# Optimization experiments

Hardware: AMD Instinct MI355X
Metric: run time of the kernel (lower is better)

## Reference

```python
import jax, jax.numpy as jnp
import numpy as np

N = 5000        # graph nodes
DEG = 16        # fixed out-degree -> 1-hop neighborhood size S = DEG+1
S = DEG + 1
T = 10          # n_templates
MN = 10         # n_templates_nodes
D = 128         # n_features
EPS = 0.1       # entropic regularization of the OT solver
N_OUTER = 3     # FGW outer (gradient/linearization) iterations
N_SINK = 5      # Sinkhorn projections per outer iteration


def setup_inputs() -> dict:
    key = jax.random.key(0)
    k1, k2, k3, k4 = jax.random.split(key, 4)
    x = jax.random.normal(k1, (N, D), jnp.float32)
    dst = jax.random.randint(k2, (N * DEG,), 0, N)
    src = jnp.repeat(jnp.arange(N), DEG)
    edge_index = jnp.stack([src, dst])  # [2, E], node i's neighbors are rows i*DEG:(i+1)*DEG
    tmpl = jax.random.uniform(k3, (T, MN, MN), jnp.float32)
    templates = 0.5 * (tmpl + jnp.swapaxes(tmpl, 1, 2))  # symmetric init, as in template_initialisation
    templates_features = 0.001 * jax.random.normal(k4, (T, MN, D), jnp.float32)
    q0 = jnp.zeros((T, MN), jnp.float32)
    alpha0 = jnp.zeros((1,), jnp.float32)
    return {"x": x, "edge_index": edge_index, "templates": templates,
            "templates_features": templates_features, "q0": q0, "alpha0": alpha0}


def _ltfgw(x, edge_index, templates, templates_features, q0, alpha0):
    alpha = jax.nn.sigmoid(alpha0)[0]
    C2 = jax.nn.softmax(templates, axis=1)        # [T,m,m] template structure (softmax over dim=1 as in forward)
    q = jax.nn.softmax(q0, axis=1)                # [T,m] template node weights
    dst = edge_index[1].reshape(N, DEG)           # neighbor list per node
    nodes_local = jnp.concatenate([jnp.arange(N)[:, None], dst], axis=1)  # [N,S] 1-hop neighborhood
    # local adjacency C1[n,a,b] = 1 iff edge between local nodes a,b (symmetrized, no self loop)
    neigh_all = dst[nodes_local]                  # [N,S,DEG]
    adj = (neigh_all[:, :, None, :] == nodes_local[:, None, :, None]).any(-1)
    adj = adj | jnp.swapaxes(adj, 1, 2)
    C1 = adj.astype(x.dtype) * (1.0 - jnp.eye(S, dtype=x.dtype))
    p = jnp.full((S,), 1.0 / S, dtype=x.dtype)    # uniform local node weights
    F2 = templates_features
    xl = x[nodes_local]                           # [N,S,D]
    # feature cost M[n,t,s,m] = ||xl[n,s] - F2[t,m]||^2
    M = ((xl ** 2).sum(-1)[:, None, :, None] + (F2 ** 2).sum(-1)[None, :, None, :]
         - 2.0 * jnp.einsum('nsd,tmd->ntsm', xl, F2))
    # GW (square loss) constant terms
    hC1 = jnp.einsum('nij,j->ni', C1 ** 2, p)
    hC2 = jnp.einsum('tij,tj->ti', C2 ** 2, q)
    constC = hC1[:, None, :, None] + hC2[None, :, None, :]   # [N,T,S,m]
    log_p = jnp.log(p)[None, None, :]
    log_q = jnp.log(q)[None, :, :]
    G = (p[None, None, :, None] * q[None, :, None, :]) * jnp.ones((N, 1, 1, 1), x.dtype)

    def outer(G, _):
        tens = constC - 2.0 * jnp.einsum('nij,ntjk,tlk->ntil', C1, G, C2)
        cost = (1.0 - alpha) * M + 2.0 * alpha * tens        # FGW gradient = linearized cost
        logK = -cost / EPS
        def sink(ab, _):
            a, b = ab
            a = log_p - jax.nn.logsumexp(logK + b[:, :, None, :], axis=-1)
            b = log_q - jax.nn.logsumexp(logK + a[..., None], axis=-2)
            return (a, b), None
        init = (jnp.zeros((N, T, S), x.dtype), jnp.zeros((N, T, MN), x.dtype))
        (a, b), _ = jax.lax.scan(sink, init, None, length=N_SINK)
        return jnp.exp(logK + a[..., None] + b[:, :, None, :]), None

    G, _ = jax.lax.scan(outer, G, None, length=N_OUTER)
    tens = constC - 2.0 * jnp.einsum('nij,ntjk,tlk->ntil', C1, G, C2)
    # FGW value per (node, template): (1-a)<M,G> + a<constC - 2 C1 G C2^T, G>
    dist = jnp.sum(G * ((1.0 - alpha) * M + alpha * tens), axis=(-2, -1))
    return dist  # [N, T]


def reference(x, edge_index, templates, templates_features, q0, alpha0):
    return _ltfgw(x, edge_index, templates, templates_features, q0, alpha0)
```

## Files before the change

kernel.cpp:

```cpp
#include <hip/hip_runtime.h>
#include <math.h>

#define NN   5000
#define DEG  16
#define S    17
#define T    10
#define MN   10
#define D    128
#define NOUT 3
#define NSK  5

#define WPB   8
#define BLOCK (WPB * 64)
#define NEG   -3.0e38f
#define LOG2E 1.44269504088896f
#define LN2   0.69314718055995f
#define TINY  1e-30f

typedef unsigned uint2v __attribute__((ext_vector_type(2)));

__device__ __forceinline__ float fast_rcp(float x) { return __builtin_amdgcn_rcpf(x); }

#if __has_builtin(__builtin_amdgcn_exp2f)
__device__ __forceinline__ float fast_exp2(float x) { return __builtin_amdgcn_exp2f(x); }
#else
__device__ __forceinline__ float fast_exp2(float x) { return __expf(x * LN2); }
#endif

template <int CTRL>
__device__ __forceinline__ float dpp_movf(float v) {
    return __int_as_float(__builtin_amdgcn_update_dpp(
        0, __float_as_int(v), CTRL, 0xF, 0xF, true));
}
__device__ __forceinline__ float rowsum16(float v) {
    v += dpp_movf<0x121>(v);
    v += dpp_movf<0x122>(v);
    v += dpp_movf<0x124>(v);
    v += dpp_movf<0x128>(v);
    return v;
}
__device__ __forceinline__ float rowmax16(float v) {
    v = fmaxf(v, dpp_movf<0x121>(v));
    v = fmaxf(v, dpp_movf<0x122>(v));
    v = fmaxf(v, dpp_movf<0x124>(v));
    v = fmaxf(v, dpp_movf<0x128>(v));
    return v;
}

__device__ __forceinline__ float bfly16(float v) {
#if __has_builtin(__builtin_amdgcn_permlane16_swap)
    uint2v r = __builtin_amdgcn_permlane16_swap(__float_as_uint(v), __float_as_uint(v),
                                                false, false);
    return __uint_as_float(r[0]) + __uint_as_float(r[1]);
#else
    return v + __int_as_float(__builtin_amdgcn_ds_swizzle(__float_as_int(v), 0x401F));
#endif
}
__device__ __forceinline__ float bfly32(float v) {
#if __has_builtin(__builtin_amdgcn_permlane32_swap)
    uint2v r = __builtin_amdgcn_permlane32_swap(__float_as_uint(v), __float_as_uint(v),
                                                false, false);
    return __uint_as_float(r[0]) + __uint_as_float(r[1]);
#else
    return v + __shfl_xor(v, 32, 64);
#endif
}

__device__ __forceinline__ float dot10(const float* __restrict__ row,
                                       const float* __restrict__ cr) {
    float4 a = *(const float4*)(row);
    float4 b = *(const float4*)(row + 4);
    float2 c = *(const float2*)(row + 8);
    float e0 = fmaf(cr[1], a.y, cr[0] * a.x);
    float e1 = fmaf(cr[3], a.w, cr[2] * a.z);
    float e2 = fmaf(cr[5], b.y, cr[4] * b.x);
    float e3 = fmaf(cr[7], b.w, cr[6] * b.z);
    float e4 = fmaf(cr[9], c.y, cr[8] * c.x);
    return ((e0 + e1) + (e2 + e3)) + e4;
}

__global__ __launch_bounds__(320) void ltfgw_pre(
    const float* __restrict__ x,
    const int*   __restrict__ edge,
    const float* __restrict__ F2,
    float*       __restrict__ wsMp,
    unsigned*    __restrict__ wsMask,
    float*       __restrict__ wsSqF2)
{
    const int n   = blockIdx.x;
    const int tid = threadIdx.x;
    const int* dst = edge + NN * DEG;

    if (n == NN) {
        if (tid < T * MN) {
            const float4* fr = (const float4*)(F2 + (size_t)tid * D);
            float acc = 0.f;
            #pragma unroll 8
            for (int i = 0; i < D / 4; ++i) {
                float4 f = fr[i];
                acc += f.x*f.x + f.y*f.y + f.z*f.z + f.w*f.w;
            }
            wsSqF2[tid] = acc;
        }
        return;
    }

    __shared__ int      loc[S];
    __shared__ int      neigh[S][DEG];
    __shared__ unsigned cm[S];
    __shared__ float    xsq_s;

    if (tid < S) { loc[tid] = (tid == 0) ? n : dst[n * DEG + tid - 1]; cm[tid] = 0u; }
    __syncthreads();

    if (tid < S * DEG) neigh[tid >> 4][tid & 15] = dst[loc[tid >> 4] * DEG + (tid & 15)];
    if (tid < 64) {
        float v0 = x[(size_t)n * D + tid];
        float v1 = x[(size_t)n * D + 64 + tid];
        float pp = v0 * v0 + v1 * v1;
        pp = rowsum16(pp);
        pp += __shfl_xor(pp, 16, 64);
        pp += __shfl_xor(pp, 32, 64);
        if (tid == 0) xsq_s = pp;
    }
    __syncthreads();

    if (tid < S * S) {
        int a = tid / S, b = tid % S;
        int la = loc[a], lb = loc[b];
        bool adj = false;
        #pragma unroll
        for (int k = 0; k < DEG; ++k) adj = adj | (neigh[a][k] == lb) | (neigh[b][k] == la);
        if (a != b && adj) atomicOr(&cm[a], 1u << b);
    }
    __syncthreads();

    if (tid < S) wsMask[n * S + tid] = cm[tid];
    if (tid >= 32 && tid < 32 + T * MN) {
        int c = tid - 32;
        const float4* fr = (const float4*)(F2 + (size_t)c * D);
        const float4* xr = (const float4*)(x + (size_t)n * D);
        float dotv = 0.f;
        #pragma unroll 8
        for (int d4 = 0; d4 < D / 4; ++d4) {
            float4 f = fr[d4], xv = xr[d4];
            dotv += f.x*xv.x + f.y*xv.y + f.z*xv.z + f.w*xv.w;
        }
        wsMp[n * (T * MN) + c] = xsq_s - 2.f * dotv;
    }
}

__global__ __launch_bounds__(BLOCK) void ltfgw_wave(
    const int*      __restrict__ edge,
    const float*    __restrict__ tmpl,
    const float*    __restrict__ q0,
    const float*    __restrict__ alpha0,
    const float*    __restrict__ wsMp,
    const unsigned* __restrict__ wsMask,
    const float*    __restrict__ wsSqF2,
    float*          __restrict__ out)
{
    const int tid  = threadIdx.x;
    const int w    = tid >> 6;
    const int gid  = blockIdx.x * WPB + w;
    const int n    = gid / T;
    const int t    = gid - n * T;
    const int lane = tid & 63;
    const int q    = lane >> 4;
    const int m    = lane & 15;
    const bool act = (m < MN);
    const int mc   = act ? m : (MN - 1);

    __shared__ __align__(16) float C2l[WPB][MN][17];
    __shared__ __align__(16) float GL[WPB][19][16];
    __shared__ __align__(16) float QL[WPB][16];

    const int* dst = edge + NN * DEG;

    float vq = q0[t * MN + mc];
    float zq = act ? vq : NEG;
    float mq = rowmax16(zq);
    float sq = rowsum16(__expf(zq - mq));
    const float qm = __expf(vq - (mq + __logf(sq)));
    if (q == 0) QL[w][m] = act ? qm : 0.f;
    if (act && q == 0) {
        float v[MN]; float cmx = NEG;
        #pragma unroll
        for (int i = 0; i < MN; ++i) { v[i] = tmpl[t * MN * MN + i * MN + m]; cmx = fmaxf(cmx, v[i]); }
        float ssum = 0.f;
        #pragma unroll
        for (int i = 0; i < MN; ++i) { v[i] = __expf(v[i] - cmx); ssum += v[i]; }
        float inv = fast_rcp(ssum);
        #pragma unroll
        for (int i = 0; i < MN; ++i) C2l[w][i][m] = v[i] * inv;
    }

    int sr[5];
    #pragma unroll
    for (int r = 0; r < 5; ++r) { int s0 = q + 4 * r; sr[r] = (s0 > 16) ? 16 : s0; }
    unsigned msk[5]; float npop[5]; float Mp[5];
    const int cidx = t * MN + mc;
    #pragma unroll
    for (int r = 0; r < 5; ++r) {
        int lr  = (sr[r] == 0) ? n : dst[n * DEG + sr[r] - 1];
        msk[r]  = wsMask[n * S + sr[r]];
        npop[r] = (float)__popc(msk[r]);
        Mp[r]   = wsMp[lr * (T * MN) + cidx];
    }
    const float sqf2c = wsSqF2[cidx];

    float crReg[MN];
    #pragma unroll
    for (int k = 0; k < MN; ++k) crReg[k] = C2l[w][mc][k];

    float hC2 = 0.f, qC2m = 0.f;
    {
        float ql[MN];
        #pragma unroll
        for (int k = 0; k < MN; ++k) ql[k] = QL[w][k];
        #pragma unroll
        for (int k = 0; k < MN; ++k) {
            float cq = crReg[k] * ql[k];
            qC2m += cq;
            hC2  = fmaf(crReg[k], cq, hC2);
        }
    }

    const float alpha = fast_rcp(1.f + __expf(-alpha0[0]));
    const float oma   = 1.f - alpha;
    const float p_    = 1.f / (float)S;
    const float fa42  = 40.f * alpha * LOG2E;
    const float qop   = qm * (float)S;
    const unsigned exm = act ? 0x1FFFEu : 0u;
    const int j16  = (q == 0) ? 16 : 18;

    float lkP2b[5], rm2[5];
    {
        const float nl2e10 = -10.f * LOG2E;
        #pragma unroll
        for (int r = 0; r < 5; ++r) {
            float M_ = Mp[r] + sqf2c;
            float cC = npop[r] * p_ + hC2;
            float lk2 = nl2e10 * (oma * M_ + 2.f * alpha * cC);
            rm2[r]   = rowmax16(act ? lk2 : NEG) + 14.4f;
            lkP2b[r] = act ? (lk2 - rm2[r]) : NEG;
        }
    }

    float tens[5], Kt[5], ub[5], v_, G[5];
    {
        float pq = p_ * qC2m;
        #pragma unroll
        for (int r = 0; r < 5; ++r) tens[r] = pq * npop[r];
    }

    for (int o = 1; o <= NOUT; ++o) {
        #pragma unroll
        for (int r = 0; r < 5; ++r)
            Kt[r] = fast_exp2(fmaf(fa42, tens[r], lkP2b[r]));
        float Kt4c = (q == 0) ? Kt[4] : 0.f;

        #pragma unroll
        for (int r = 0; r < 5; ++r) ub[r] = fast_rcp(rowsum16(Kt[r]));
        {
            float a0 = Kt[0] * ub[0], a1 = Kt[1] * ub[1];
            float a2 = Kt[2] * ub[2], a3 = Kt[3] * ub[3];
            float a4 = fmaf(Kt4c, ub[4], TINY);
            float cs = ((a0 + a1) + (a2 + a3)) + a4;
            cs = bfly16(cs); cs = bfly32(cs);
            v_ = qop * fast_rcp(cs);
        }
        #pragma unroll
        for (int it = 1; it < NSK; ++it) {
            #pragma unroll
            for (int r = 0; r < 5; ++r)
                ub[r] = fast_rcp(rowsum16(Kt[r] * v_));
            float a0 = Kt[0] * ub[0], a1 = Kt[1] * ub[1];
            float a2 = Kt[2] * ub[2], a3 = Kt[3] * ub[3];
            float a4 = fmaf(Kt4c, ub[4], TINY);
            float cs = ((a0 + a1) + (a2 + a3)) + a4;
            cs = bfly16(cs); cs = bfly32(cs);
            v_ = qop * fast_rcp(cs);
        }
        float pv = p_ * v_;
        #pragma unroll
        for (int r = 0; r < 5; ++r) G[r] = Kt[r] * ub[r] * pv;

        #pragma unroll
        for (int r = 0; r < 4; ++r) GL[w][q + 4*r][m] = G[r];
        GL[w][j16][m] = G[4];
        float cg = (G[0] + G[1]) + (G[2] + G[3]) + ((q == 0) ? G[4] : 0.f);
        cg = bfly16(cg); cg = bfly32(cg);
        if (q == 0) GL[w][17][m] = cg;
        float Fm = dot10(&GL[w][17][0], crReg);
        float H0 = dot10(&GL[w][0][0],  crReg);
        #pragma unroll
        for (int r = 0; r < 5; ++r) {
            unsigned ex = msk[r] & exm;
            if (r == 0) ex = (q == 0) ? 0u : ex;
            float tn = H0;
            while (ex) {
                int j = __builtin_ctz(ex);
                ex &= ex - 1u;
                tn += dot10(&GL[w][j][0], crReg);
            }
            tens[r] = tn;
        }
        if (q == 0) tens[0] = Fm - H0;
    }

    float val = 0.f;
    #pragma unroll
    for (int r = 0; r < 5; ++r) {
        float cC = npop[r] * p_ + hC2;
        float lk2r = lkP2b[r] + rm2[r];
        float integ = -(0.1f * LN2) * lk2r - alpha * cC - 2.f * alpha * tens[r];
        bool valid = act && (r < 4 || q == 0);
        val += valid ? G[r] * integ : 0.f;
    }
    val = rowsum16(val);
    val = bfly16(val);
    val = bfly32(val);
    if (lane == 0) out[n * T + t] = val;
}

extern "C" void kernel_launch(void* const* d_in, const int* in_sizes, int n_in,
                              void* d_out, int out_size, void* d_ws, size_t ws_size,
                              hipStream_t stream) {
    const float* x      = (const float*)d_in[0];
    const int*   edge   = (const int*)  d_in[1];
    const float* tmpl   = (const float*)d_in[2];
    const float* F2     = (const float*)d_in[3];
    const float* q0     = (const float*)d_in[4];
    const float* alpha0 = (const float*)d_in[5];
    float*       out    = (float*)d_out;

    float*    wsMp    = (float*)d_ws;
    unsigned* wsMask  = (unsigned*)((char*)d_ws + (size_t)NN * T * MN * 4);
    float*    wsSqF2  = (float*)((char*)d_ws + (size_t)NN * T * MN * 4 + (size_t)NN * S * 4);

    hipLaunchKernelGGL(ltfgw_pre, dim3(NN + 1), dim3(320), 0, stream,
                       x, edge, F2, wsMp, wsMask, wsSqF2);
    hipLaunchKernelGGL(ltfgw_wave, dim3(NN * T / WPB), dim3(BLOCK), 0, stream,
                       edge, tmpl, q0, alpha0, wsMp, wsMask, wsSqF2, out);
}
```

Measured before the change: 219.3 us.

## Pack two node-template problems per wavefront using 32-lane halves

Each 64-lane wavefront now solves two (node, template) FGW problems, one per 32-lane half, with 9 rows per lane instead of 5. The grid is halved and cross-lane reductions drop the 32-lane butterfly step. The row-max values are moved into shared memory to save registers. The cost is more registers per lane for the larger row arrays and a longer serial chain of work per lane, which can lower occupancy.

```diff
diff --git a/kernel.cpp b/kernel.cpp
--- a/kernel.cpp
+++ b/kernel.cpp
@@ -11,7 +11,9 @@
 #define NSK  5
 
 #define WPB   8
+#define PPW   2
 #define BLOCK (WPB * 64)
+#define RS    9
 #define NEG   -3.0e38f
 #define LOG2E 1.44269504088896f
 #define LN2   0.69314718055995f
@@ -54,15 +56,6 @@
     return __uint_as_float(r[0]) + __uint_as_float(r[1]);
 #else
     return v + __int_as_float(__builtin_amdgcn_ds_swizzle(__float_as_int(v), 0x401F));
-#endif
-}
-__device__ __forceinline__ float bfly32(float v) {
-#if __has_builtin(__builtin_amdgcn_permlane32_swap)
-    uint2v r = __builtin_amdgcn_permlane32_swap(__float_as_uint(v), __float_as_uint(v),
-                                                false, false);
-    return __uint_as_float(r[0]) + __uint_as_float(r[1]);
-#else
-    return v + __shfl_xor(v, 32, 64);
 #endif
 }
 
@@ -162,18 +155,22 @@
 {
     const int tid  = threadIdx.x;
     const int w    = tid >> 6;
-    const int gid  = blockIdx.x * WPB + w;
-    const int n    = gid / T;
-    const int t    = gid - n * T;
     const int lane = tid & 63;
+    const int half = lane >> 5;
     const int q    = lane >> 4;
+    const int ql   = q & 1;
     const int m    = lane & 15;
     const bool act = (m < MN);
     const int mc   = act ? m : (MN - 1);
-
-    __shared__ __align__(16) float C2l[WPB][MN][17];
-    __shared__ __align__(16) float GL[WPB][19][16];
-    __shared__ __align__(16) float QL[WPB][16];
+    const bool pad8 = (ql == 1);
+    const int gid  = (blockIdx.x * WPB + w) * PPW + half;
+    const int n    = gid / T;
+    const int t    = gid - n * T;
+
+    __shared__ __align__(16) float C2l[WPB][PPW][MN][17];
+    __shared__ __align__(16) float GL [WPB][PPW][19][16];
+    __shared__ __align__(16) float QL [WPB][PPW][16];
+    __shared__               float RM [WPB][PPW][20];
 
     const int* dst = edge + NN * DEG;
 
@@ -182,8 +179,8 @@
     float mq = rowmax16(zq);
     float sq = rowsum16(__expf(zq - mq));
     const float qm = __expf(vq - (mq + __logf(sq)));
-    if (q == 0) QL[w][m] = act ? qm : 0.f;
-    if (act && q == 0) {
+    if (ql == 0) QL[w][half][m] = act ? qm : 0.f;
+    if (act && ql == 0) {
         float v[MN]; float cmx = NEG;
         #pragma unroll
         for (int i = 0; i < MN; ++i) { v[i] = tmpl[t * MN * MN + i * MN + m]; cmx = fmaxf(cmx, v[i]); }
@@ -192,35 +189,33 @@
         for (int i = 0; i < MN; ++i) { v[i] = __expf(v[i] - cmx); ssum += v[i]; }
         float inv = fast_rcp(ssum);
         #pragma unroll
-        for (int i = 0; i < MN; ++i) C2l[w][i][m] = v[i] * inv;
-    }
-
-    int sr[5];
-    #pragma unroll
-    for (int r = 0; r < 5; ++r) { int s0 = q + 4 * r; sr[r] = (s0 > 16) ? 16 : s0; }
-    unsigned msk[5]; float npop[5]; float Mp[5];
+        for (int i = 0; i < MN; ++i) C2l[w][half][i][m] = v[i] * inv;
+    }
+
+    unsigned msk[RS]; float Mp[RS];
     const int cidx = t * MN + mc;
     #pragma unroll
-    for (int r = 0; r < 5; ++r) {
-        int lr  = (sr[r] == 0) ? n : dst[n * DEG + sr[r] - 1];
-        msk[r]  = wsMask[n * S + sr[r]];
-        npop[r] = (float)__popc(msk[r]);
+    for (int r = 0; r < RS; ++r) {
+        int s   = 2 * r + ql; s = (s > 16) ? 16 : s;
+        int lr  = (s == 0) ? n : dst[n * DEG + s - 1];
+        msk[r]  = wsMask[n * S + s];
         Mp[r]   = wsMp[lr * (T * MN) + cidx];
     }
+    if (pad8) msk[8] = 0u;
     const float sqf2c = wsSqF2[cidx];
 
     float crReg[MN];
     #pragma unroll
-    for (int k = 0; k < MN; ++k) crReg[k] = C2l[w][mc][k];
+    for (int k = 0; k < MN; ++k) crReg[k] = C2l[w][half][mc][k];
 
     float hC2 = 0.f, qC2m = 0.f;
     {
-        float ql[MN];
-        #pragma unroll
-        for (int k = 0; k < MN; ++k) ql[k] = QL[w][k];
+        float ql_[MN];
+        #pragma unroll
+        for (int k = 0; k < MN; ++k) ql_[k] = QL[w][half][k];
         #pragma unroll
         for (int k = 0; k < MN; ++k) {
-            float cq = crReg[k] * ql[k];
+            float cq = crReg[k] * ql_[k];
             qC2m += cq;
             hC2  = fmaf(crReg[k], cq, hC2);
         }
@@ -232,96 +227,100 @@
     const float fa42  = 40.f * alpha * LOG2E;
     const float qop   = qm * (float)S;
     const unsigned exm = act ? 0x1FFFEu : 0u;
-    const int j16  = (q == 0) ? 16 : 18;
-
-    float lkP2b[5], rm2[5];
+
+    float lkP2b[RS];
     {
         const float nl2e10 = -10.f * LOG2E;
         #pragma unroll
-        for (int r = 0; r < 5; ++r) {
-            float M_ = Mp[r] + sqf2c;
-            float cC = npop[r] * p_ + hC2;
+        for (int r = 0; r < RS; ++r) {
+            int s = 2 * r + ql; s = (s > 16) ? 16 : s;
+            float M_  = Mp[r] + sqf2c;
+            float cC  = (float)__popc(msk[r]) * p_ + hC2;
             float lk2 = nl2e10 * (oma * M_ + 2.f * alpha * cC);
-            rm2[r]   = rowmax16(act ? lk2 : NEG) + 14.4f;
-            lkP2b[r] = act ? (lk2 - rm2[r]) : NEG;
-        }
-    }
-
-    float tens[5], Kt[5], ub[5], v_, G[5];
+            float rm2 = rowmax16(act ? lk2 : NEG) + 14.4f;
+            bool vld  = !(pad8 && r == 8);
+            lkP2b[r]  = (act && vld) ? (lk2 - rm2) : NEG;
+            if (m == 0 && vld) RM[w][half][s] = rm2;
+        }
+    }
+
+    float tens[RS], Kt[RS], ub[RS], v_, G[RS];
     {
         float pq = p_ * qC2m;
         #pragma unroll
-        for (int r = 0; r < 5; ++r) tens[r] = pq * npop[r];
+        for (int r = 0; r < RS; ++r) tens[r] = pq * (float)__popc(msk[r]);
     }
 
     for (int o = 1; o <= NOUT; ++o) {
         #pragma unroll
-        for (int r = 0; r < 5; ++r)
+        for (int r = 0; r < RS; ++r)
             Kt[r] = fast_exp2(fmaf(fa42, tens[r], lkP2b[r]));
-        float Kt4c = (q == 0) ? Kt[4] : 0.f;
-
-        #pragma unroll
-        for (int r = 0; r < 5; ++r) ub[r] = fast_rcp(rowsum16(Kt[r]));
+
+        #pragma unroll
+        for (int r = 0; r < RS; ++r) ub[r] = fast_rcp(rowsum16(Kt[r]));
         {
-            float a0 = Kt[0] * ub[0], a1 = Kt[1] * ub[1];
-            float a2 = Kt[2] * ub[2], a3 = Kt[3] * ub[3];
-            float a4 = fmaf(Kt4c, ub[4], TINY);
-            float cs = ((a0 + a1) + (a2 + a3)) + a4;
-            cs = bfly16(cs); cs = bfly32(cs);
+            float a8  = Kt[8] * ub[8];
+            float a8g = pad8 ? 0.f : a8;
+            float cs  = (((Kt[0]*ub[0] + Kt[1]*ub[1]) + (Kt[2]*ub[2] + Kt[3]*ub[3]))
+                       + ((Kt[4]*ub[4] + Kt[5]*ub[5]) + (Kt[6]*ub[6] + Kt[7]*ub[7])))
+                       + (a8g + TINY);
+            cs = bfly16(cs);
             v_ = qop * fast_rcp(cs);
         }
         #pragma unroll
         for (int it = 1; it < NSK; ++it) {
             #pragma unroll
-            for (int r = 0; r < 5; ++r)
+            for (int r = 0; r < RS; ++r)
                 ub[r] = fast_rcp(rowsum16(Kt[r] * v_));
-            float a0 = Kt[0] * ub[0], a1 = Kt[1] * ub[1];
-            float a2 = Kt[2] * ub[2], a3 = Kt[3] * ub[3];
-            float a4 = fmaf(Kt4c, ub[4], TINY);
-            float cs = ((a0 + a1) + (a2 + a3)) + a4;
-            cs = bfly16(cs); cs = bfly32(cs);
+            float a8  = Kt[8] * ub[8];
+            float a8g = pad8 ? 0.f : a8;
+            float cs  = (((Kt[0]*ub[0] + Kt[1]*ub[1]) + (Kt[2]*ub[2] + Kt[3]*ub[3]))
+                       + ((Kt[4]*ub[4] + Kt[5]*ub[5]) + (Kt[6]*ub[6] + Kt[7]*ub[7])))
+                       + (a8g + TINY);
+            cs = bfly16(cs);
             v_ = qop * fast_rcp(cs);
         }
         float pv = p_ * v_;
         #pragma unroll
-        for (int r = 0; r < 5; ++r) G[r] = Kt[r] * ub[r] * pv;
-
-        #pragma unroll
-        for (int r = 0; r < 4; ++r) GL[w][q + 4*r][m] = G[r];
-        GL[w][j16][m] = G[4];
-        float cg = (G[0] + G[1]) + (G[2] + G[3]) + ((q == 0) ? G[4] : 0.f);
-        cg = bfly16(cg); cg = bfly32(cg);
-        if (q == 0) GL[w][17][m] = cg;
-        float Fm = dot10(&GL[w][17][0], crReg);
-        float H0 = dot10(&GL[w][0][0],  crReg);
-        #pragma unroll
-        for (int r = 0; r < 5; ++r) {
+        for (int r = 0; r < RS; ++r) G[r] = Kt[r] * ub[r] * pv;
+
+        #pragma unroll
+        for (int r = 0; r < 8; ++r) GL[w][half][2*r + ql][m] = G[r];
+        GL[w][half][pad8 ? 18 : 16][m] = G[8];
+        float cg = (((G[0]+G[1]) + (G[2]+G[3])) + ((G[4]+G[5]) + (G[6]+G[7])))
+                 + (pad8 ? 0.f : G[8]);
+        cg = bfly16(cg);
+        if (ql == 0) GL[w][half][17][m] = cg;
+        float Fm = dot10(&GL[w][half][17][0], crReg);
+        float H0 = dot10(&GL[w][half][0][0],  crReg);
+        #pragma unroll
+        for (int r = 0; r < RS; ++r) {
             unsigned ex = msk[r] & exm;
-            if (r == 0) ex = (q == 0) ? 0u : ex;
+            if (r == 0) ex = (ql == 0) ? 0u : ex;
             float tn = H0;
             while (ex) {
                 int j = __builtin_ctz(ex);
                 ex &= ex - 1u;
-                tn += dot10(&GL[w][j][0], crReg);
+                tn += dot10(&GL[w][half][j][0], crReg);
             }
             tens[r] = tn;
         }
-        if (q == 0) tens[0] = Fm - H0;
+        if (ql == 0) tens[0] = Fm - H0;
     }
 
     float val = 0.f;
     #pragma unroll
-    for (int r = 0; r < 5; ++r) {
-        float cC = npop[r] * p_ + hC2;
-        float lk2r = lkP2b[r] + rm2[r];
+    for (int r = 0; r < RS; ++r) {
+        int s = 2 * r + ql; s = (s > 16) ? 16 : s;
+        float cC   = (float)__popc(msk[r]) * p_ + hC2;
+        float lk2r = lkP2b[r] + RM[w][half][s];
         float integ = -(0.1f * LN2) * lk2r - alpha * cC - 2.f * alpha * tens[r];
-        bool valid = act && (r < 4 || q == 0);
+        bool valid = act && !(pad8 && r == 8);
         val += valid ? G[r] * integ : 0.f;
     }
     val = rowsum16(val);
     val = bfly16(val);
-    val = bfly32(val);
-    if (lane == 0) out[n * T + t] = val;
+    if ((lane & 31) == 0) out[gid] = val;
 }
 
 extern "C" void kernel_launch(void* const* d_in, const int* in_sizes, int n_in,
@@ -341,6 +340,6 @@
 
     hipLaunchKernelGGL(ltfgw_pre, dim3(NN + 1), dim3(320), 0, stream,
                        x, edge, F2, wsMp, wsMask, wsSqF2);
-    hipLaunchKernelGGL(ltfgw_wave, dim3(NN * T / WPB), dim3(BLOCK), 0, stream,
+    hipLaunchKernelGGL(ltfgw_wave, dim3(NN * T / (WPB * PPW)), dim3(BLOCK), 0, stream,
                        edge, tmpl, q0, alpha0, wsMp, wsMask, wsSqF2, out);
 }
```

After: 200.8 us. 1.09x faster.
